# Optimization experiments

Measured on AMD Instinct MI355X. Metric: run time of the kernel, lower is better.

Reference implementation:

```python
import jax, jax.numpy as jnp
import numpy as np
from jax import lax

B, T, D = 4096, 2048, 10
H = 4          # num_units
OUT = 30       # output_dim


def setup_inputs() -> dict:
    key = jax.random.key(0)
    ks = jax.random.split(key, 7)
    s_ih = 1.0 / np.sqrt(H)
    return {
        "X": jax.random.normal(ks[0], (B, T, D), dtype=jnp.float32),
        # PyTorch LSTM params, gate order (i, f, g, o)
        "W_ih": jax.random.uniform(ks[1], (4 * H, D), minval=-s_ih, maxval=s_ih, dtype=jnp.float32),
        "W_hh": jax.random.uniform(ks[2], (4 * H, H), minval=-s_ih, maxval=s_ih, dtype=jnp.float32),
        "b_ih": jax.random.uniform(ks[3], (4 * H,), minval=-s_ih, maxval=s_ih, dtype=jnp.float32),
        "b_hh": jax.random.uniform(ks[4], (4 * H,), minval=-s_ih, maxval=s_ih, dtype=jnp.float32),
        "W_out": jax.random.uniform(ks[5], (OUT, H), minval=-s_ih, maxval=s_ih, dtype=jnp.float32),
        "b_out": jax.random.uniform(ks[6], (OUT,), minval=-s_ih, maxval=s_ih, dtype=jnp.float32),
    }


def _lstm_last_hidden(X, W_ih, W_hh, b_ih, b_hh):
    # Precompute input projections for all timesteps: [B, T, 4H]
    x_proj = jnp.einsum('btd,gd->btg', X, W_ih) + b_ih + b_hh
    h0 = jnp.zeros((X.shape[0], W_hh.shape[1]), dtype=X.dtype)
    c0 = jnp.zeros_like(h0)

    def step(carry, xt):  # xt: [B, 4H]
        h, c = carry
        gates = xt + h @ W_hh.T
        i, f, g, o = jnp.split(gates, 4, axis=-1)
        i = jax.nn.sigmoid(i)
        f = jax.nn.sigmoid(f)
        g = jnp.tanh(g)
        o = jax.nn.sigmoid(o)
        c = f * c + i * g
        h = o * jnp.tanh(c)
        return (h, c), None

    (h_T, _), _ = lax.scan(step, (h0, c0), jnp.swapaxes(x_proj, 0, 1))
    return h_T  # [B, H]


def reference(X, W_ih, W_hh, b_ih, b_hh, W_out, b_out):
    h_T = _lstm_last_hidden(X, W_ih, W_hh, b_ih, b_hh)
    # dropout p=0 is a no-op; softmax over output_dim
    logits = h_T @ W_out.T + b_out
    return jax.nn.softmax(logits, axis=-1)
```

## Files before the change

### kernel.cpp

```cpp
#include <hip/hip_runtime.h>
#include <stdint.h>

#define B_TOT 4096
#define T_LEN 2048
#define D_IN  10
#define OUT_N 30
#define CSTEP 32
#define NCH   (T_LEN/CSTEP)
#define SMP_BLK 16
#define XBUF_F (CSTEP*SMP_BLK*D_IN)
#define ABUF_F (CSTEP*SMP_BLK*16)
#define NLD   (XBUF_F/(4*64))
#define CH_BYTES (CSTEP*D_IN*4)

#define GLD4(gptr, lptr) __builtin_amdgcn_global_load_lds( \
    (const __attribute__((address_space(1))) void*)(gptr),  \
    (__attribute__((address_space(3))) void*)(lptr), 4, 0, 0)

template<int CTRL>
__device__ __forceinline__ float dppf(float x) {
    return __int_as_float(
        __builtin_amdgcn_mov_dpp(__float_as_int(x), CTRL, 0xF, 0xF, true));
}

__device__ __forceinline__ float fast_exp2(float x) {
#if __has_builtin(__builtin_amdgcn_exp2f)
    return __builtin_amdgcn_exp2f(x);
#else
    float r; asm("v_exp_f32 %0, %1" : "=v"(r) : "v"(x)); return r;
#endif
}

__launch_bounds__(512, 2)
__global__ void lstm_scan_kernel(const float* __restrict__ X,
                                 const float* __restrict__ W_ih,
                                 const float* __restrict__ W_hh,
                                 const float* __restrict__ b_ih,
                                 const float* __restrict__ b_hh,
                                 float* __restrict__ hT)
{
    __shared__ float xbuf[2][XBUF_F];
    __shared__ float abuf[2][ABUF_F];

    const int tid  = threadIdx.x;
    const int lane = tid & 63;
    const int w    = tid >> 6;
    const int lr   = lane & 15;
    const int grp  = lane >> 4;
    const int u    = (lr >> 2) & 3;
    const int tau  = lr & 3;
    const int rw   = tau * 4 + u;
    const uint32_t samp0 = (uint32_t)blockIdx.x * SMP_BLK;

    const float KT = -2.8853900817779268f;
    const float KS = -1.4426950408889634f;
    const float mneg = (tau == 2) ? KT : KS;

    if (w >= 4) {
        const int pw = w - 4;
        const int sg = pw * 4 + grp;
        float wih[10];
        #pragma unroll
        for (int d0 = 0; d0 < 10; ++d0) wih[d0] = W_ih[rw*10 + d0] * mneg;
        const float bsum = (b_ih[rw] + b_hh[rw]) * mneg;

        uint32_t voff[NLD];
        #pragma unroll
        for (int kk = 0; kk < NLD; ++kk) {
            int p   = (pw*NLD + kk)*64 + lane;
            int t   = p / 160;
            int rem = p - t*160;
            int s   = rem / 10;
            int d0  = rem - s*10;
            voff[kk] = (samp0 + (uint32_t)s) * (uint32_t)(T_LEN*D_IN*4)
                     + (uint32_t)(t*40 + d0*4);
        }
        const char* Xc = (const char*)X;

        auto produce = [&](int bb) {
            #pragma unroll 4
            for (int t = 0; t < CSTEP; ++t) {
                const float2* xp =
                    (const float2*)&xbuf[bb][(t*SMP_BLK + sg)*10];
                float2 x0 = xp[0], x1 = xp[1], x2 = xp[2],
                       x3 = xp[3], x4 = xp[4];
                float acc = bsum;
                acc = fmaf(wih[0], x0.x, acc); acc = fmaf(wih[1], x0.y, acc);
                acc = fmaf(wih[2], x1.x, acc); acc = fmaf(wih[3], x1.y, acc);
                acc = fmaf(wih[4], x2.x, acc); acc = fmaf(wih[5], x2.y, acc);
                acc = fmaf(wih[6], x3.x, acc); acc = fmaf(wih[7], x3.y, acc);
                acc = fmaf(wih[8], x4.x, acc); acc = fmaf(wih[9], x4.y, acc);
                abuf[bb][(t*SMP_BLK + sg)*16 + lr] = acc;
            }
        };

        #pragma unroll
        for (int kk = 0; kk < NLD; ++kk)
            GLD4(Xc + voff[kk], &xbuf[0][(pw*NLD+kk)*64]);
        __syncthreads();
        #pragma unroll
        for (int kk = 0; kk < NLD; ++kk)
            GLD4(Xc + (voff[kk] + CH_BYTES), &xbuf[1][(pw*NLD+kk)*64]);
        produce(0);
        __syncthreads();

        for (int k = 0; k < NCH; ++k) {
            if (k + 1 < NCH) {
                if (k + 2 < NCH) {
                    const uint32_t add = (uint32_t)(k+2) * CH_BYTES;
                    #pragma unroll
                    for (int kk = 0; kk < NLD; ++kk)
                        GLD4(Xc + (voff[kk] + add),
                             &xbuf[k&1][(pw*NLD+kk)*64]);
                }
                produce((k+1)&1);
            }
            __syncthreads();
        }
    } else {
        __builtin_amdgcn_s_setprio(1);
        const int sg = w * 4 + grp;
        const float k1 = (tau == 0) ? KT : ((tau == 1) ? 1.0f : 2.0f);
        const float k0 = (tau == 2) ? -1.0f : 0.0f;
        const float whhA = W_hh[rw*4 +  u        ] * mneg;
        const float whhB = W_hh[rw*4 + ((u+3)&3)] * mneg;
        const float whhC = W_hh[rw*4 + ((u+2)&3)] * mneg;
        const float whhD = W_hh[rw*4 + ((u+1)&3)] * mneg;

        __syncthreads();
        __syncthreads();

        float cs = 0.f, hown = 0.f;
        for (int k = 0; k < NCH; ++k) {
            const float* ab = &abuf[k&1][sg*16 + lr];
            float xr[CSTEP];
            #pragma unroll
            for (int t = 0; t < CSTEP; ++t) xr[t] = ab[t*256];
            #pragma unroll
            for (int t = 0; t < CSTEP; ++t) {
                float hB = dppf<0x124>(hown);
                float hC = dppf<0x128>(hown);
                float hD = dppf<0x12C>(hown);
                float u1 = fmaf(whhA, hown, xr[t]);
                float acc = fmaf(whhB, hB, u1) + fmaf(whhD, hD, whhC * hC);
                float e  = fast_exp2(acc);
                float a  = fmaf(k1, __builtin_amdgcn_rcpf(1.0f + e), k0);
                float gi = dppf<0x00>(a);
                float gf = dppf<0x55>(a);
                float gg = dppf<0xAA>(a);
                float go = dppf<0xFF>(a);
                float mgo = -0.5f * go;
                cs = fmaf(gf, cs, gi * gg);
                float e2 = fast_exp2(cs);
                float r2 = __builtin_amdgcn_rcpf(1.0f + e2);
                hown = fmaf(go, r2, mgo);
            }
            __syncthreads();
        }
        if (tau == 0) hT[(samp0 + sg)*4 + u] = hown;
    }
}

__global__ void head_kernel(const float* __restrict__ hT,
                            const float* __restrict__ W_out,
                            const float* __restrict__ b_out,
                            float* __restrict__ out)
{
    int b = blockIdx.x * blockDim.x + threadIdx.x;
    if (b >= B_TOT) return;
    float4 h = ((const float4*)hT)[b];
    float lg[OUT_N];
    float m = -1e30f;
    #pragma unroll
    for (int o = 0; o < OUT_N; ++o) {
        float v = b_out[o];
        v = fmaf(W_out[o*4+0], h.x, v);
        v = fmaf(W_out[o*4+1], h.y, v);
        v = fmaf(W_out[o*4+2], h.z, v);
        v = fmaf(W_out[o*4+3], h.w, v);
        lg[o] = v;
        m = fmaxf(m, v);
    }
    float s = 0.f;
    #pragma unroll
    for (int o = 0; o < OUT_N; ++o) {
        float e = fast_exp2((lg[o] - m) * 1.4426950408889634f);
        lg[o] = e;
        s += e;
    }
    float rs = 1.0f / s;
    #pragma unroll
    for (int o = 0; o < OUT_N; ++o) out[(size_t)b*OUT_N + o] = lg[o] * rs;
}

extern "C" void kernel_launch(void* const* d_in, const int* in_sizes, int n_in,
                              void* d_out, int out_size, void* d_ws, size_t ws_size,
                              hipStream_t stream)
{
    const float* X     = (const float*)d_in[0];
    const float* W_ih  = (const float*)d_in[1];
    const float* W_hh  = (const float*)d_in[2];
    const float* b_ih  = (const float*)d_in[3];
    const float* b_hh  = (const float*)d_in[4];
    const float* W_out = (const float*)d_in[5];
    const float* b_out = (const float*)d_in[6];
    float* out = (float*)d_out;
    float* hTs = (float*)d_ws;

    lstm_scan_kernel<<<B_TOT/SMP_BLK, 512, 0, stream>>>(X, W_ih, W_hh, b_ih, b_hh, hTs);
    head_kernel<<<B_TOT/256, 256, 0, stream>>>(hTs, W_out, b_out, out);
}
```

Measured before the change: 251.3 us.

## Interleave two LSTM samples per lane and halve block size

Each consumer lane now advances two independent LSTM recurrences (A and B) in lockstep, and each producer lane computes two input projections. The block shrinks from 512 to 256 threads (2 consumer and 2 producer waves) while keeping 16 samples per block. The aim is instruction-level parallelism that hides the latency of the serial dependency chain of DPP, exp and rcp. The abuf row stride is padded to 17 to reduce LDS bank conflicts, and per-step LDS reads replace the register prefetch array. The trade-off is fewer waves per block and more register pressure per lane, under changed launch bounds.

```diff
diff --git a/kernel.cpp b/kernel.cpp
--- a/kernel.cpp
+++ b/kernel.cpp
@@ -8,9 +8,10 @@
 #define CSTEP 32
 #define NCH   (T_LEN/CSTEP)
 #define SMP_BLK 16
+#define ASTR  17
 #define XBUF_F (CSTEP*SMP_BLK*D_IN)
-#define ABUF_F (CSTEP*SMP_BLK*16)
-#define NLD   (XBUF_F/(4*64))
+#define ABUF_F (CSTEP*SMP_BLK*ASTR)
+#define NLDW  (XBUF_F/(2*64))
 #define CH_BYTES (CSTEP*D_IN*4)
 
 #define GLD4(gptr, lptr) __builtin_amdgcn_global_load_lds( \
@@ -31,7 +32,7 @@
 #endif
 }
 
-__launch_bounds__(512, 2)
+__launch_bounds__(256, 1)
 __global__ void lstm_scan_kernel(const float* __restrict__ X,
                                  const float* __restrict__ W_ih,
                                  const float* __restrict__ W_hh,
@@ -46,7 +47,6 @@
     const int lane = tid & 63;
     const int w    = tid >> 6;
     const int lr   = lane & 15;
-    const int grp  = lane >> 4;
     const int u    = (lr >> 2) & 3;
     const int tau  = lr & 3;
     const int rw   = tau * 4 + u;
@@ -56,18 +56,20 @@
     const float KS = -1.4426950408889634f;
     const float mneg = (tau == 2) ? KT : KS;
 
-    if (w >= 4) {
-        const int pw = w - 4;
-        const int sg = pw * 4 + grp;
+    if (w >= 2) {
+        const int pw = w - 2;
+        const int sp = lane >> 4;
+        const int pA = pw * 8 + sp * 2;
+        const int pB = pA + 1;
         float wih[10];
         #pragma unroll
         for (int d0 = 0; d0 < 10; ++d0) wih[d0] = W_ih[rw*10 + d0] * mneg;
         const float bsum = (b_ih[rw] + b_hh[rw]) * mneg;
 
-        uint32_t voff[NLD];
-        #pragma unroll
-        for (int kk = 0; kk < NLD; ++kk) {
-            int p   = (pw*NLD + kk)*64 + lane;
+        uint32_t voff[NLDW];
+        #pragma unroll
+        for (int kk = 0; kk < NLDW; ++kk) {
+            int p   = (pw*NLDW + kk)*64 + lane;
             int t   = p / 160;
             int rem = p - t*160;
             int s   = rem / 10;
@@ -80,27 +82,33 @@
         auto produce = [&](int bb) {
             #pragma unroll 4
             for (int t = 0; t < CSTEP; ++t) {
-                const float2* xp =
-                    (const float2*)&xbuf[bb][(t*SMP_BLK + sg)*10];
-                float2 x0 = xp[0], x1 = xp[1], x2 = xp[2],
-                       x3 = xp[3], x4 = xp[4];
-                float acc = bsum;
-                acc = fmaf(wih[0], x0.x, acc); acc = fmaf(wih[1], x0.y, acc);
-                acc = fmaf(wih[2], x1.x, acc); acc = fmaf(wih[3], x1.y, acc);
-                acc = fmaf(wih[4], x2.x, acc); acc = fmaf(wih[5], x2.y, acc);
-                acc = fmaf(wih[6], x3.x, acc); acc = fmaf(wih[7], x3.y, acc);
-                acc = fmaf(wih[8], x4.x, acc); acc = fmaf(wih[9], x4.y, acc);
-                abuf[bb][(t*SMP_BLK + sg)*16 + lr] = acc;
+                const float2* xa = (const float2*)&xbuf[bb][(t*SMP_BLK + pA)*10];
+                const float2* xb = (const float2*)&xbuf[bb][(t*SMP_BLK + pB)*10];
+                float2 a0 = xa[0], a1 = xa[1], a2 = xa[2], a3 = xa[3], a4 = xa[4];
+                float2 b0 = xb[0], b1 = xb[1], b2 = xb[2], b3 = xb[3], b4 = xb[4];
+                float accA = bsum, accB = bsum;
+                accA = fmaf(wih[0], a0.x, accA); accB = fmaf(wih[0], b0.x, accB);
+                accA = fmaf(wih[1], a0.y, accA); accB = fmaf(wih[1], b0.y, accB);
+                accA = fmaf(wih[2], a1.x, accA); accB = fmaf(wih[2], b1.x, accB);
+                accA = fmaf(wih[3], a1.y, accA); accB = fmaf(wih[3], b1.y, accB);
+                accA = fmaf(wih[4], a2.x, accA); accB = fmaf(wih[4], b2.x, accB);
+                accA = fmaf(wih[5], a2.y, accA); accB = fmaf(wih[5], b2.y, accB);
+                accA = fmaf(wih[6], a3.x, accA); accB = fmaf(wih[6], b3.x, accB);
+                accA = fmaf(wih[7], a3.y, accA); accB = fmaf(wih[7], b3.y, accB);
+                accA = fmaf(wih[8], a4.x, accA); accB = fmaf(wih[8], b4.x, accB);
+                accA = fmaf(wih[9], a4.y, accA); accB = fmaf(wih[9], b4.y, accB);
+                abuf[bb][(t*SMP_BLK + pA)*ASTR + lr] = accA;
+                abuf[bb][(t*SMP_BLK + pB)*ASTR + lr] = accB;
             }
         };
 
         #pragma unroll
-        for (int kk = 0; kk < NLD; ++kk)
-            GLD4(Xc + voff[kk], &xbuf[0][(pw*NLD+kk)*64]);
-        __syncthreads();
-        #pragma unroll
-        for (int kk = 0; kk < NLD; ++kk)
-            GLD4(Xc + (voff[kk] + CH_BYTES), &xbuf[1][(pw*NLD+kk)*64]);
+        for (int kk = 0; kk < NLDW; ++kk)
+            GLD4(Xc + voff[kk], &xbuf[0][(pw*NLDW+kk)*64]);
+        __syncthreads();
+        #pragma unroll
+        for (int kk = 0; kk < NLDW; ++kk)
+            GLD4(Xc + (voff[kk] + CH_BYTES), &xbuf[1][(pw*NLDW+kk)*64]);
         produce(0);
         __syncthreads();
 
@@ -109,9 +117,9 @@
                 if (k + 2 < NCH) {
                     const uint32_t add = (uint32_t)(k+2) * CH_BYTES;
                     #pragma unroll
-                    for (int kk = 0; kk < NLD; ++kk)
+                    for (int kk = 0; kk < NLDW; ++kk)
                         GLD4(Xc + (voff[kk] + add),
-                             &xbuf[k&1][(pw*NLD+kk)*64]);
+                             &xbuf[k&1][(pw*NLDW+kk)*64]);
                 }
                 produce((k+1)&1);
             }
@@ -119,7 +127,9 @@
         }
     } else {
         __builtin_amdgcn_s_setprio(1);
-        const int sg = w * 4 + grp;
+        const int grp = lane >> 4;
+        const int sgA = w * 8 + grp * 2;
+        const int sgB = sgA + 1;
         const float k1 = (tau == 0) ? KT : ((tau == 1) ? 1.0f : 2.0f);
         const float k0 = (tau == 2) ? -1.0f : 0.0f;
         const float whhA = W_hh[rw*4 +  u        ] * mneg;
@@ -130,34 +140,46 @@
         __syncthreads();
         __syncthreads();
 
-        float cs = 0.f, hown = 0.f;
+        float csA = 0.f, hsA = 0.f;
+        float csB = 0.f, hsB = 0.f;
         for (int k = 0; k < NCH; ++k) {
-            const float* ab = &abuf[k&1][sg*16 + lr];
-            float xr[CSTEP];
-            #pragma unroll
-            for (int t = 0; t < CSTEP; ++t) xr[t] = ab[t*256];
+            const float* aA = &abuf[k&1][sgA*ASTR + lr];
+            const float* aB = &abuf[k&1][sgB*ASTR + lr];
             #pragma unroll
             for (int t = 0; t < CSTEP; ++t) {
-                float hB = dppf<0x124>(hown);
-                float hC = dppf<0x128>(hown);
-                float hD = dppf<0x12C>(hown);
-                float u1 = fmaf(whhA, hown, xr[t]);
-                float acc = fmaf(whhB, hB, u1) + fmaf(whhD, hD, whhC * hC);
-                float e  = fast_exp2(acc);
-                float a  = fmaf(k1, __builtin_amdgcn_rcpf(1.0f + e), k0);
-                float gi = dppf<0x00>(a);
-                float gf = dppf<0x55>(a);
-                float gg = dppf<0xAA>(a);
-                float go = dppf<0xFF>(a);
-                float mgo = -0.5f * go;
-                cs = fmaf(gf, cs, gi * gg);
-                float e2 = fast_exp2(cs);
-                float r2 = __builtin_amdgcn_rcpf(1.0f + e2);
-                hown = fmaf(go, r2, mgo);
+                float xA = aA[t*(SMP_BLK*ASTR)];
+                float xB = aB[t*(SMP_BLK*ASTR)];
+                float hBA = dppf<0x124>(hsA);   float hBB = dppf<0x124>(hsB);
+                float hCA = dppf<0x128>(hsA);   float hCB = dppf<0x128>(hsB);
+                float hDA = dppf<0x12C>(hsA);   float hDB = dppf<0x12C>(hsB);
+                float u1A = fmaf(whhA, hsA, xA);
+                float u1B = fmaf(whhA, hsB, xB);
+                float acA = fmaf(whhB, hBA, u1A) + fmaf(whhD, hDA, whhC * hCA);
+                float acB = fmaf(whhB, hBB, u1B) + fmaf(whhD, hDB, whhC * hCB);
+                float eA  = fast_exp2(acA);
+                float eB  = fast_exp2(acB);
+                float aAv = fmaf(k1, __builtin_amdgcn_rcpf(1.0f + eA), k0);
+                float aBv = fmaf(k1, __builtin_amdgcn_rcpf(1.0f + eB), k0);
+                float giA = dppf<0x00>(aAv);    float giB = dppf<0x00>(aBv);
+                float gfA = dppf<0x55>(aAv);    float gfB = dppf<0x55>(aBv);
+                float ggA = dppf<0xAA>(aAv);    float ggB = dppf<0xAA>(aBv);
+                float goA = dppf<0xFF>(aAv);    float goB = dppf<0xFF>(aBv);
+                float mgoA = -0.5f * goA;       float mgoB = -0.5f * goB;
+                csA = fmaf(gfA, csA, giA * ggA);
+                csB = fmaf(gfB, csB, giB * ggB);
+                float e2A = fast_exp2(csA);
+                float e2B = fast_exp2(csB);
+                float r2A = __builtin_amdgcn_rcpf(1.0f + e2A);
+                float r2B = __builtin_amdgcn_rcpf(1.0f + e2B);
+                hsA = fmaf(goA, r2A, mgoA);
+                hsB = fmaf(goB, r2B, mgoB);
             }
             __syncthreads();
         }
-        if (tau == 0) hT[(samp0 + sg)*4 + u] = hown;
+        if (tau == 0) {
+            hT[(samp0 + sgA)*4 + u] = hsA;
+            hT[(samp0 + sgB)*4 + u] = hsB;
+        }
     }
 }
 
@@ -207,6 +229,6 @@
     float* out = (float*)d_out;
     float* hTs = (float*)d_ws;
 
-    lstm_scan_kernel<<<B_TOT/SMP_BLK, 512, 0, stream>>>(X, W_ih, W_hh, b_ih, b_hh, hTs);
+    lstm_scan_kernel<<<B_TOT/SMP_BLK, 256, 0, stream>>>(X, W_ih, W_hh, b_ih, b_hh, hTs);
     head_kernel<<<B_TOT/256, 256, 0, stream>>>(hTs, W_out, b_out, out);
 }
```

New measurement: 388.0 us. 1.54x slower.
